# Kernel optimization log

Hardware: AMD Instinct MI355X
Metric: run time of the kernel (lower is better)

Reference implementation:

```python
import jax, jax.numpy as jnp
import numpy as np

EPSILON = 0.1
NUM_STAB = 1e-4


def setup_inputs() -> dict:
    key = jax.random.key(0)
    k1, k2, k3 = jax.random.split(key, 3)
    B, C, H, Wd = 1024, 3, 32, 32
    n = C * H * Wd          # 3072 input dims
    c = 10                  # classes
    data = jax.random.normal(k1, (B, C, H, Wd), dtype=jnp.float32)
    # stand-in differentiable classifier (linear) so the Jacobian wrt data is defined
    W = jax.random.normal(k2, (n, c), dtype=jnp.float32) * 0.02
    b = jax.random.normal(k3, (c,), dtype=jnp.float32) * 0.02
    return {"data": data, "W": W, "b": b}


def reference(data, W, b):
    B = data.shape[0]
    n = data.shape[1] * data.shape[2] * data.shape[3]
    c = W.shape[1]
    m = c - 1

    def new_coord_fn(x):  # x: [C,H,W] single sample
        logits = x.reshape(-1) @ W + b                              # [c]
        probs = jax.nn.softmax(logits) * (1 - c * NUM_STAB) + NUM_STAB
        r = jnp.sqrt(probs)
        return 2.0 * r[:m] / (1.0 - r[m])                           # [m]

    # batched Jacobian replaces the per-class autograd.grad loop: [B, m, C, H, W]
    jac = jax.vmap(jax.jacrev(new_coord_fn))(data).reshape(B, m, n)
    G = jnp.einsum('bik,bjk->bij', jac, jac)                        # [B, m, m]

    logits = data.reshape(B, -1) @ W + b                            # [B, c]
    probs = jax.nn.softmax(logits, axis=1) * (1 - c * NUM_STAB) + NUM_STAB
    coeff = 4.0 * (1.0 - jnp.sqrt(probs[:, m])) ** 2                # [B]
    delta = 2.0 * jnp.arccos(jnp.sqrt(probs / c).sum(axis=1))       # [B]
    factor = (delta ** 2 / coeff / EPSILON ** 2)[:, None, None]     # [B,1,1]

    diff = G - factor * jnp.eye(m, dtype=G.dtype)[None]
    reg = jnp.linalg.norm(diff.reshape(B, -1), axis=1) / n          # [B]
    return (reg.mean(), jnp.array(0))
```

## Files before the change

kernel.cpp:

```cpp
#include <hip/hip_runtime.h>
#include <math.h>

#define NDIM   3072
#define C10    10
#define M9     9
#define SYM55  55
#define SPB    2
#define NCHUNK 3

__global__ __launch_bounds__(256) void wtw_kernel(const float* __restrict__ W,
                                                  float* __restrict__ ws) {
    __shared__ float s_red[4][64];
    const int t = threadIdx.x;
    const int lane = t & 63, wid = t >> 6;
    const int k = blockIdx.x * 256 + t;

    float w[C10];
#pragma unroll
    for (int j = 0; j < C10; ++j) w[j] = W[k * C10 + j];

    float g[64];
#pragma unroll
    for (int i = 0; i < 64; ++i) g[i] = 0.f;
    {
        int idx = 0;
#pragma unroll
        for (int a = 0; a < C10; ++a)
#pragma unroll
            for (int b = a; b < C10; ++b) { g[idx] = w[a] * w[b]; ++idx; }
    }

#pragma unroll
    for (int step = 32; step >= 1; step >>= 1) {
#pragma unroll
        for (int i = 0; i < step; ++i) {
            float keep = (lane & step) ? g[i + step] : g[i];
            float send = (lane & step) ? g[i] : g[i + step];
            g[i] = keep + __shfl_xor(send, step);
        }
    }
    s_red[wid][lane] = g[0];
    __syncthreads();
    if (t < SYM55)
        atomicAdd(&ws[t], s_red[0][t] + s_red[1][t] + s_red[2][t] + s_red[3][t]);
}

__global__ __launch_bounds__(256, 2) void iso_fused(const float* __restrict__ data,
                                                    const float* __restrict__ W,
                                                    const float* __restrict__ bias,
                                                    const float* __restrict__ Msym,
                                                    float* __restrict__ out,
                                                    int B, float inv_scale,
                                                    int out_size) {
    __shared__ float s_red[4][SPB * C10];
    __shared__ float s_M[C10 * C10];
    __shared__ float s_logit[SPB][C10];
    __shared__ float s_p[SPB][C10];
    __shared__ float s_r[SPB][C10];
    __shared__ float s_u[SPB];
    __shared__ float s_fac[SPB];
    __shared__ float s_A[SPB][M9 * C10];
    __shared__ float s_T[SPB][M9 * C10];
    __shared__ float s_sq[SPB][M9 * M9];
    __shared__ float s_part[SPB];

    const int t = threadIdx.x;
    const int lane = t & 63, wid = t >> 6;
    const int sbase = blockIdx.x * SPB;

    float g0[64];
#pragma unroll
    for (int i = 0; i < 64; ++i) g0[i] = 0.f;

    const float4* Wq = (const float4*)W;
    const float4* dq = (const float4*)data;
    int xbase[SPB];
#pragma unroll
    for (int s = 0; s < SPB; ++s) {
        int sidx = sbase + s; if (sidx >= B) sidx = B - 1;
        xbase[s] = sidx * (NDIM / 4);
    }

#pragma unroll 1
    for (int c = 0; c < NCHUNK; ++c) {
        const int kb = (c << 8) | t;
        float w[40];
#pragma unroll
        for (int p = 0; p < 10; ++p) {
            float4 v = Wq[kb * 10 + p];
            w[4 * p + 0] = v.x; w[4 * p + 1] = v.y;
            w[4 * p + 2] = v.z; w[4 * p + 3] = v.w;
        }
        float x[SPB][4];
#pragma unroll
        for (int s = 0; s < SPB; ++s) {
            float4 v = dq[xbase[s] + kb];
            x[s][0] = v.x; x[s][1] = v.y; x[s][2] = v.z; x[s][3] = v.w;
        }
#pragma unroll
        for (int kk = 0; kk < 4; ++kk)
#pragma unroll
            for (int s = 0; s < SPB; ++s)
#pragma unroll
                for (int j = 0; j < C10; ++j)
                    g0[s * C10 + j] = fmaf(x[s][kk], w[kk * 10 + j], g0[s * C10 + j]);
    }

#pragma unroll
    for (int step = 32; step >= 1; step >>= 1) {
#pragma unroll
        for (int i = 0; i < step; ++i) {
            float keep = (lane & step) ? g0[i + step] : g0[i];
            float send = (lane & step) ? g0[i] : g0[i + step];
            g0[i] = keep + __shfl_xor(send, step);
        }
    }
    if (lane < SPB * C10) s_red[wid][lane] = g0[0];
    __syncthreads();

    if (t < SPB * C10) {
        float v = s_red[0][t] + s_red[1][t] + s_red[2][t] + s_red[3][t];
        s_logit[t / C10][t % C10] = v + bias[t % C10];
    }
    if (t >= 64 && t < 64 + SYM55) {
        int e = t - 64;
        float v = Msym[e];
        int a = 0, rem = e;
        while (rem >= C10 - a) { rem -= C10 - a; ++a; }
        int b = a + rem;
        s_M[a * C10 + b] = v;
        s_M[b * C10 + a] = v;
    }
    __syncthreads();

    if (t < SPB) {
        float lg[C10];
#pragma unroll
        for (int j = 0; j < C10; ++j) lg[j] = s_logit[t][j];
        float mx = lg[0];
#pragma unroll
        for (int j = 1; j < C10; ++j) mx = fmaxf(mx, lg[j]);
        float ex[C10], sum = 0.f;
#pragma unroll
        for (int j = 0; j < C10; ++j) { ex[j] = expf(lg[j] - mx); sum += ex[j]; }
        float inv = 1.f / sum;
        float ssq = 0.f;
#pragma unroll
        for (int j = 0; j < C10; ++j) {
            float p = ex[j] * inv;
            float q = fmaf(p, 0.999f, 1e-4f);
            float r = sqrtf(q);
            s_p[t][j] = p;
            s_r[t][j] = r;
            ssq += sqrtf(q * 0.1f);
        }
        ssq = fminf(ssq, 1.0f);
        float delta = 2.f * acosf(ssq);
        float rm = s_r[t][M9];
        float omr = 1.f - rm;
        float u = 1.f / omr;
        float coeff = 4.f * omr * omr;
        s_u[t] = u;
        s_fac[t] = delta * delta / (coeff * (0.1f * 0.1f));
    }
    __syncthreads();

    for (int e = t; e < SPB * M9 * C10; e += 256) {
        int s = e / (M9 * C10), rem = e % (M9 * C10);
        int i = rem / C10, j = rem % C10;
        float u = s_u[s];
        float pi = s_p[s][i], ri = s_r[s][i];
        float p9 = s_p[s][M9], r9 = s_r[s][M9];
        float alpha = u * 0.999f * pi / ri;
        float beta  = u * u * 0.999f * ri * p9 / r9;
        float a = -(alpha + beta) * s_p[s][j];
        if (j == i)  a += alpha;
        if (j == M9) a += beta;
        s_A[s][rem] = a;
    }
    __syncthreads();

    for (int e = t; e < SPB * M9 * C10; e += 256) {
        int s = e / (M9 * C10), rem = e % (M9 * C10);
        int i = rem / C10, b = rem % C10;
        float sum = 0.f;
#pragma unroll
        for (int j = 0; j < C10; ++j) sum = fmaf(s_A[s][i * C10 + j], s_M[j * C10 + b], sum);
        s_T[s][rem] = sum;
    }
    __syncthreads();

    for (int e = t; e < SPB * M9 * M9; e += 256) {
        int s = e / (M9 * M9), rem = e % (M9 * M9);
        int i = rem / M9, k = rem % M9;
        float g = 0.f;
#pragma unroll
        for (int b = 0; b < C10; ++b) g = fmaf(s_T[s][i * C10 + b], s_A[s][k * C10 + b], g);
        float d = g - ((i == k) ? s_fac[s] : 0.f);
        s_sq[s][rem] = d * d;
    }
    __syncthreads();

    if (t < SPB) {
        int sidx = sbase + t;
        float sum = 0.f;
#pragma unroll
        for (int r = 0; r < M9 * M9; ++r) sum += s_sq[t][r];
        s_part[t] = (sidx < B) ? sqrtf(sum) : 0.f;
    }
    __syncthreads();

    if (t == 0) {
        float part = 0.f;
#pragma unroll
        for (int s = 0; s < SPB; ++s) part += s_part[s];
        atomicAdd(out, part * inv_scale);
        if (blockIdx.x == 0 && out_size > 1) out[1] = 0.f;
    }
}

extern "C" void kernel_launch(void* const* d_in, const int* in_sizes, int n_in,
                              void* d_out, int out_size, void* d_ws, size_t ws_size,
                              hipStream_t stream) {
    const float* data = (const float*)d_in[0];
    const float* W    = (const float*)d_in[1];
    const float* bias = (const float*)d_in[2];
    float* out = (float*)d_out;
    float* ws  = (float*)d_ws;
    const int B = in_sizes[0] / NDIM;
    const int nblocks = (B + SPB - 1) / SPB;
    const float inv_scale = 1.0f / ((float)NDIM * (float)B);

    hipMemsetAsync(ws, 0, SYM55 * sizeof(float), stream);
    wtw_kernel<<<NDIM / 256, 256, 0, stream>>>(W, ws);
    iso_fused<<<nblocks, 256, 0, stream>>>(data, W, bias, ws, out, B, inv_scale, out_size);
}
```

Measured before the change: 83.54 us.

## Fold W^T W Gram computation into the fused per-sample kernel

Removes the separate wtw_kernel and its workspace memset. Each block of the main kernel now recomputes the 55 symmetric entries of W^T W alongside the logits, reusing the W values it already loads. This drops one launch, the atomics and the global workspace round-trip. In exchange every block repeats the full W^T W accumulation, adding 55 FMAs per k, extra registers and an 11-value shuffle reduction.

```diff
diff --git a/kernel.cpp b/kernel.cpp
--- a/kernel.cpp
+++ b/kernel.cpp
@@ -8,51 +8,14 @@
 #define SPB    2
 #define NCHUNK 3
 
-__global__ __launch_bounds__(256) void wtw_kernel(const float* __restrict__ W,
-                                                  float* __restrict__ ws) {
-    __shared__ float s_red[4][64];
-    const int t = threadIdx.x;
-    const int lane = t & 63, wid = t >> 6;
-    const int k = blockIdx.x * 256 + t;
-
-    float w[C10];
-#pragma unroll
-    for (int j = 0; j < C10; ++j) w[j] = W[k * C10 + j];
-
-    float g[64];
-#pragma unroll
-    for (int i = 0; i < 64; ++i) g[i] = 0.f;
-    {
-        int idx = 0;
-#pragma unroll
-        for (int a = 0; a < C10; ++a)
-#pragma unroll
-            for (int b = a; b < C10; ++b) { g[idx] = w[a] * w[b]; ++idx; }
-    }
-
-#pragma unroll
-    for (int step = 32; step >= 1; step >>= 1) {
-#pragma unroll
-        for (int i = 0; i < step; ++i) {
-            float keep = (lane & step) ? g[i + step] : g[i];
-            float send = (lane & step) ? g[i] : g[i + step];
-            g[i] = keep + __shfl_xor(send, step);
-        }
-    }
-    s_red[wid][lane] = g[0];
-    __syncthreads();
-    if (t < SYM55)
-        atomicAdd(&ws[t], s_red[0][t] + s_red[1][t] + s_red[2][t] + s_red[3][t]);
-}
-
 __global__ __launch_bounds__(256, 2) void iso_fused(const float* __restrict__ data,
                                                     const float* __restrict__ W,
                                                     const float* __restrict__ bias,
-                                                    const float* __restrict__ Msym,
                                                     float* __restrict__ out,
                                                     int B, float inv_scale,
                                                     int out_size) {
-    __shared__ float s_red[4][SPB * C10];
+    __shared__ float s_red[4][64];
+    __shared__ float s_red1[4][11];
     __shared__ float s_M[C10 * C10];
     __shared__ float s_logit[SPB][C10];
     __shared__ float s_p[SPB][C10];
@@ -68,9 +31,11 @@
     const int lane = t & 63, wid = t >> 6;
     const int sbase = blockIdx.x * SPB;
 
-    float g0[64];
+    float g0[64], g1[11];
 #pragma unroll
     for (int i = 0; i < 64; ++i) g0[i] = 0.f;
+#pragma unroll
+    for (int i = 0; i < 11; ++i) g1[i] = 0.f;
 
     const float4* Wq = (const float4*)W;
     const float4* dq = (const float4*)data;
@@ -98,12 +63,22 @@
             x[s][0] = v.x; x[s][1] = v.y; x[s][2] = v.z; x[s][3] = v.w;
         }
 #pragma unroll
-        for (int kk = 0; kk < 4; ++kk)
+        for (int kk = 0; kk < 4; ++kk) {
 #pragma unroll
             for (int s = 0; s < SPB; ++s)
 #pragma unroll
                 for (int j = 0; j < C10; ++j)
-                    g0[s * C10 + j] = fmaf(x[s][kk], w[kk * 10 + j], g0[s * C10 + j]);
+                    g0[20 * 0 + s * C10 + j] = fmaf(x[s][kk], w[kk * 10 + j], g0[s * C10 + j]);
+            int idx = 0;
+#pragma unroll
+            for (int a = 0; a < C10; ++a)
+#pragma unroll
+                for (int b = a; b < C10; ++b) {
+                    if (idx < 44) g0[20 + idx] = fmaf(w[kk*10+a], w[kk*10+b], g0[20 + idx]);
+                    else          g1[idx - 44] = fmaf(w[kk*10+a], w[kk*10+b], g1[idx - 44]);
+                    ++idx;
+                }
+        }
     }
 
 #pragma unroll
@@ -115,7 +90,16 @@
             g0[i] = keep + __shfl_xor(send, step);
         }
     }
-    if (lane < SPB * C10) s_red[wid][lane] = g0[0];
+    s_red[wid][lane] = g0[0];
+#pragma unroll
+    for (int step = 32; step >= 1; step >>= 1)
+#pragma unroll
+        for (int v = 0; v < 11; ++v)
+            g1[v] += __shfl_xor(g1[v], step);
+    if (lane == 0) {
+#pragma unroll
+        for (int v = 0; v < 11; ++v) s_red1[wid][v] = g1[v];
+    }
     __syncthreads();
 
     if (t < SPB * C10) {
@@ -124,7 +108,9 @@
     }
     if (t >= 64 && t < 64 + SYM55) {
         int e = t - 64;
-        float v = Msym[e];
+        float v;
+        if (e < 44) v = s_red[0][20 + e] + s_red[1][20 + e] + s_red[2][20 + e] + s_red[3][20 + e];
+        else        v = s_red1[0][e - 44] + s_red1[1][e - 44] + s_red1[2][e - 44] + s_red1[3][e - 44];
         int a = 0, rem = e;
         while (rem >= C10 - a) { rem -= C10 - a; ++a; }
         int b = a + rem;
@@ -226,12 +212,9 @@
     const float* W    = (const float*)d_in[1];
     const float* bias = (const float*)d_in[2];
     float* out = (float*)d_out;
-    float* ws  = (float*)d_ws;
     const int B = in_sizes[0] / NDIM;
     const int nblocks = (B + SPB - 1) / SPB;
     const float inv_scale = 1.0f / ((float)NDIM * (float)B);
 
-    hipMemsetAsync(ws, 0, SYM55 * sizeof(float), stream);
-    wtw_kernel<<<NDIM / 256, 256, 0, stream>>>(W, ws);
-    iso_fused<<<nblocks, 256, 0, stream>>>(data, W, bias, ws, out, B, inv_scale, out_size);
+    iso_fused<<<nblocks, 256, 0, stream>>>(data, W, bias, out, B, inv_scale, out_size);
 }
```

Measured after the change: 77.70 us. 7.0% less time.
